# Optimization experiments

Hardware: AMD Instinct MI355X
Metric: run time of the kernel (lower is better)

The kernel has to match this reference:

```python
import jax, jax.numpy as jnp
import numpy as np

B, S, D = 8, 1024, 768
H = 12
HD = D // H  # 64


def setup_inputs() -> dict:
    key = jax.random.key(0)
    k1, k2, k3 = jax.random.split(key, 3)
    x = jax.random.normal(k1, (B, S, D), dtype=jnp.float32)
    W_qkv = jax.random.normal(k2, (D, 3 * D), dtype=jnp.float32) * (1.0 / np.sqrt(D))
    W_proj = jax.random.normal(k3, (D, D), dtype=jnp.float32) * (1.0 / np.sqrt(D))
    b_proj = jnp.zeros((D,), dtype=jnp.float32)
    return {"x": x, "W_qkv": W_qkv, "W_proj": W_proj, "b_proj": b_proj}


def reference(x, W_qkv, W_proj, b_proj):
    bs, seq, d = x.shape
    qkv = x @ W_qkv  # [B,S,3D]
    qkv = qkv.reshape(bs, seq, 3, H, HD).transpose(2, 0, 3, 1, 4)  # [3,B,H,S,HD]
    Q, K, V = qkv[0], qkv[1], qkv[2]
    scores = jnp.einsum("bhqd,bhkd->bhqk", Q, K)
    mask = jnp.triu(jnp.ones((seq, seq), dtype=bool), k=1)
    scores = jnp.where(mask, -jnp.inf, scores)
    # NOTE: original divides by d_k**(-0.5), i.e. MULTIPLIES by sqrt(HD) (faithful bug)
    weights = jax.nn.softmax(scores * np.sqrt(HD).astype(np.float32), axis=-1)
    out = jnp.einsum("bhqk,bhkd->bhqd", weights, V)  # [B,H,S,HD]
    out = out.transpose(0, 2, 1, 3).reshape(bs, seq, d)
    return out @ W_proj + b_proj
```

## Files before the change

### kernel.cpp

```cpp
#include <hip/hip_runtime.h>

typedef float f32x4 __attribute__((ext_vector_type(4)));
typedef unsigned short u16;
typedef __attribute__((ext_vector_type(8))) unsigned short u16x8;

__device__ __forceinline__ u16 f2bf(float f) {
  unsigned u = __float_as_uint(f);
  u += 0x7FFFu + ((u >> 16) & 1u);
  return (u16)(u >> 16);
}
__device__ __forceinline__ float bf2f(u16 h) { return __uint_as_float(((unsigned)h) << 16); }

__device__ __forceinline__ void mfma16(f32x4 a, f32x4 b, f32x4& c) {
  asm("v_mfma_f32_16x16x32_bf16 %0, %1, %2, %0" : "+v"(c) : "v"(a), "v"(b));
}

__device__ __forceinline__ void gload16(const u16* g, const u16* l) {
  __builtin_amdgcn_global_load_lds(
      (const __attribute__((address_space(1))) void*)g,
      (__attribute__((address_space(3))) void*)l, 16, 0, 0);
}

__device__ __forceinline__ size_t tiled_off(int r, int k) {
  return (size_t)(r >> 7) * 98304 + (size_t)(k >> 5) * 4096 +
         (size_t)((k & 31) >> 3) * 1024 + (size_t)(r & 127) * 8 + (k & 7);
}

__global__ __launch_bounds__(256) void prep_tile_x(const float* __restrict__ x,
                                                   u16* __restrict__ xh,
                                                   u16* __restrict__ xl) {
  const int lane = threadIdx.x & 63;
  const int wid = threadIdx.x >> 6;
  const int row = blockIdx.x * 64 + lane;
  const int ktile = blockIdx.y * 4 + wid;
  const float4* src = reinterpret_cast<const float4*>(x + (size_t)row * 768 + ktile * 32);
  float4 f[8];
#pragma unroll
  for (int i = 0; i < 8; ++i) f[i] = src[i];
  const size_t base = (size_t)(row >> 7) * 98304 + (size_t)ktile * 4096 + (size_t)(row & 127) * 8;
#pragma unroll
  for (int c = 0; c < 4; ++c) {
    const float v[8] = {f[2 * c].x, f[2 * c].y, f[2 * c].z, f[2 * c].w,
                        f[2 * c + 1].x, f[2 * c + 1].y, f[2 * c + 1].z, f[2 * c + 1].w};
    u16x8 h, l;
#pragma unroll
    for (int e = 0; e < 8; ++e) {
      const u16 hb = f2bf(v[e]);
      h[e] = hb;
      l[e] = f2bf(v[e] - bf2f(hb));
    }
    *(u16x8*)(xh + base + c * 1024) = h;
    *(u16x8*)(xl + base + c * 1024) = l;
  }
}

template <int WRITE_LO>
__global__ __launch_bounds__(256) void prep_wt(const float* __restrict__ W,
                                               u16* __restrict__ Wth,
                                               u16* __restrict__ Wtl, int Ncols) {
  int t = blockIdx.x * 256 + threadIdx.x;
  int total = Ncols * 192;
  if (t >= total) return;
  int n = t % Ncols;
  int k4 = t / Ncols;
  const int k0 = k4 * 4;
  u16 hh[4], ll[4];
#pragma unroll
  for (int j = 0; j < 4; ++j) {
    float v = W[(size_t)(k0 + j) * Ncols + n];
    hh[j] = f2bf(v);
    ll[j] = f2bf(v - bf2f(hh[j]));
  }
  const size_t dst = tiled_off(n, k0);
  ushort4 h4; h4.x = hh[0]; h4.y = hh[1]; h4.z = hh[2]; h4.w = hh[3];
  *reinterpret_cast<ushort4*>(Wth + dst) = h4;
  if (WRITE_LO) {
    ushort4 l4v; l4v.x = ll[0]; l4v.y = ll[1]; l4v.z = ll[2]; l4v.w = ll[3];
    *reinterpret_cast<ushort4*>(Wtl + dst) = l4v;
  }
}

template <int SPLIT>
__device__ __forceinline__ void gemm_core(u16* lds,
                                          const u16* __restrict__ Ah, const u16* __restrict__ Al,
                                          const u16* __restrict__ Bh, const u16* __restrict__ Bl,
                                          int Kdim, int rowBase, int colBase, f32x4 acc[4][4]) {
  const int tid = threadIdx.x;
  const int lane = tid & 63;
  const int wid = tid >> 6;
  const int wr = wid >> 1, wc = wid & 1;
  const int l15 = lane & 15, l4 = lane >> 4;
  const size_t aT = (size_t)(rowBase >> 7) * 98304;
  const size_t bT = (size_t)(colBase >> 7) * 98304;
  const int nk = Kdim >> 5;

  for (int kt = 0; kt < nk; ++kt) {
#pragma unroll
    for (int j = 0; j < 2; ++j) {
      const int i = wid * 2 + j;
      const size_t off = (size_t)kt * 4096 + i * 512 + lane * 8;
      gload16(Ah + aT + off, lds + i * 512);
      gload16(Bh + bT + off, lds + 4096 + i * 512);
      if constexpr (SPLIT) {
        gload16(Al + aT + off, lds + 8192 + i * 512);
        gload16(Bl + bT + off, lds + 12288 + i * 512);
      }
    }
    __syncthreads();

    f32x4 fah[4], fbh[4], fal[4], fbl[4];
#pragma unroll
    for (int mi = 0; mi < 4; ++mi) {
      const int row = wr * 64 + mi * 16 + l15;
      fah[mi] = *(const f32x4*)(lds + (l4 * 128 + row) * 8);
      if constexpr (SPLIT) fal[mi] = *(const f32x4*)(lds + 8192 + (l4 * 128 + row) * 8);
    }
#pragma unroll
    for (int nj = 0; nj < 4; ++nj) {
      const int col = wc * 64 + nj * 16 + l15;
      fbh[nj] = *(const f32x4*)(lds + 4096 + (l4 * 128 + col) * 8);
      if constexpr (SPLIT) fbl[nj] = *(const f32x4*)(lds + 12288 + (l4 * 128 + col) * 8);
    }
#pragma unroll
    for (int mi = 0; mi < 4; ++mi)
#pragma unroll
      for (int nj = 0; nj < 4; ++nj) {
        mfma16(fah[mi], fbh[nj], acc[mi][nj]);
        if constexpr (SPLIT) {
          mfma16(fah[mi], fbl[nj], acc[mi][nj]);
          mfma16(fal[mi], fbh[nj], acc[mi][nj]);
        }
      }
    __syncthreads();
  }
}

__global__ __launch_bounds__(256) void gemm_qkv_kernel(
    const u16* __restrict__ xh, const u16* __restrict__ xl,
    const u16* __restrict__ Wqh, const u16* __restrict__ Wql,
    u16* __restrict__ Qh, u16* __restrict__ Ql,
    u16* __restrict__ Kh, u16* __restrict__ Kl,
    u16* __restrict__ Vt) {
  __shared__ u16 lds[16384];
  const int rowBase = blockIdx.x * 128;
  const int colBase = blockIdx.y * 128;
  const int tid = threadIdx.x, lane = tid & 63, wid = tid >> 6;
  const int wr = wid >> 1, wc = wid & 1, l15 = lane & 15, l4 = lane >> 4;
  const int which = colBase / 768;
  const int cb = colBase % 768;

  f32x4 acc[4][4];
#pragma unroll
  for (int a = 0; a < 4; ++a)
#pragma unroll
    for (int b = 0; b < 4; ++b) acc[a][b] = (f32x4){0.f, 0.f, 0.f, 0.f};

  if (which == 2) {
    gemm_core<0>(lds, xh, nullptr, Wqh, nullptr, 768, rowBase, colBase, acc);
#pragma unroll
    for (int mi = 0; mi < 4; ++mi) {
#pragma unroll
      for (int nj = 0; nj < 4; ++nj) {
        const int crem = cb + wc * 64 + nj * 16 + l15;
        const int h = crem >> 6, d = crem & 63;
        const int rg0 = rowBase + wr * 64 + mi * 16 + l4 * 4;
        const int b = rg0 >> 10, s0 = rg0 & 1023;
        const int bh = b * 12 + h;
        ushort4 st;
        st.x = f2bf(acc[mi][nj][0]); st.y = f2bf(acc[mi][nj][1]);
        st.z = f2bf(acc[mi][nj][2]); st.w = f2bf(acc[mi][nj][3]);
        *reinterpret_cast<ushort4*>(Vt + (((size_t)(bh * 64 + d)) << 10) + s0) = st;
      }
    }
  } else {
    gemm_core<1>(lds, xh, xl, Wqh, Wql, 768, rowBase, colBase, acc);
    u16* dsth = (which == 0) ? Qh : Kh;
    u16* dstl = (which == 0) ? Ql : Kl;
#pragma unroll
    for (int mi = 0; mi < 4; ++mi) {
#pragma unroll
      for (int nj = 0; nj < 4; ++nj) {
        const int crem = cb + wc * 64 + nj * 16 + l15;
        const int h = crem >> 6, d = crem & 63;
        const int rg0 = rowBase + wr * 64 + mi * 16 + l4 * 4;
        const int b = rg0 >> 10, s0 = rg0 & 1023;
        const int bh = b * 12 + h;
#pragma unroll
        for (int r = 0; r < 4; ++r) {
          const float v = acc[mi][nj][r];
          const size_t idx = ((((size_t)bh) << 10) + s0 + r) * 64 + d;
          const u16 hb = f2bf(v);
          dsth[idx] = hb;
          dstl[idx] = f2bf(v - bf2f(hb));
        }
      }
    }
  }
}

__global__ __launch_bounds__(512, 4) void attn_kernel(
    const u16* __restrict__ Qh, const u16* __restrict__ Ql,
    const u16* __restrict__ Kh, const u16* __restrict__ Kl,
    const u16* __restrict__ Vt, u16* __restrict__ attnO) {
  const int pair = blockIdx.x;
  const int bh = blockIdx.y;
  const int tid = threadIdx.x, lane = tid & 63, w = tid >> 6;
  const int l15 = lane & 15, l4 = lane >> 4;
  __shared__ u16 kv[2][12288];
  __shared__ u16 plds[8][1024];
  u16* pl = plds[w];

  const int qt0 = pair, qt1 = 7 - pair;
  const int n0 = 2 * qt0 + 2;
  const int ntot = 18;

  const int srow = lane >> 3;
  const int schunk = (lane & 7) ^ srow;
  const int krow = w * 8 + srow;

  f32x4 qfh[2], qfl[2], o[4];
  float m[4], ls[4];

#define STAGE(BSEL, KT)                                                                   \
  do {                                                                                    \
    u16* buf_ = kv[(BSEL)];                                                               \
    const size_t kgo = (size_t)(bh * 1024 + (KT) * 64 + krow) * 64 + schunk * 8;          \
    gload16(Kh + kgo, buf_ + w * 512);                                                    \
    gload16(Kl + kgo, buf_ + 4096 + w * 512);                                             \
    gload16(Vt + (size_t)(bh * 64 + krow) * 1024 + (KT) * 64 + schunk * 8,                \
            buf_ + 8192 + w * 512);                                                       \
  } while (0)

  STAGE(0, 0);

  for (int i = 0; i < ntot; ++i) {
    const int seg = (i >= n0) ? 1 : 0;
    const int kt = seg ? (i - n0) : i;
    const int qt = seg ? qt1 : qt0;
    const int qb = qt * 128 + w * 16;
    const int nseg = seg ? (ntot - n0) : n0;

    if (i + 1 < ntot) {
      const int seg2 = (i + 1 >= n0) ? 1 : 0;
      const int kt2 = seg2 ? (i + 1 - n0) : (i + 1);
      STAGE((i + 1) & 1, kt2);
      asm volatile("s_waitcnt vmcnt(3)" ::: "memory");
    } else {
      asm volatile("s_waitcnt vmcnt(0)" ::: "memory");
    }
    __builtin_amdgcn_s_barrier();

    if (kt == 0) {
#pragma unroll
      for (int ks = 0; ks < 2; ++ks) {
        const size_t off = ((size_t)(bh * 1024 + qb + l15)) * 64 + ks * 32 + l4 * 8;
        qfh[ks] = *(const f32x4*)(Qh + off);
        qfl[ks] = *(const f32x4*)(Ql + off);
      }
#pragma unroll
      for (int n = 0; n < 4; ++n) o[n] = (f32x4){0.f, 0.f, 0.f, 0.f};
#pragma unroll
      for (int r = 0; r < 4; ++r) { m[r] = -1e30f; ls[r] = 0.f; }
    }

    if (kt * 64 <= qb + 15) {
      const u16* buf = kv[i & 1];
      f32x4 sv[4];
#pragma unroll
      for (int n = 0; n < 4; ++n) sv[n] = (f32x4){0.f, 0.f, 0.f, 0.f};
      const int rsw = l15 & 7;
#pragma unroll
      for (int nt = 0; nt < 4; ++nt) {
        const int row = nt * 16 + l15;
#pragma unroll
        for (int ks = 0; ks < 2; ++ks) {
          const int kc = ks * 4 + l4;
          const int off = row * 64 + ((kc ^ rsw) << 3);
          f32x4 kfh = *(const f32x4*)(buf + off);
          f32x4 kfl = *(const f32x4*)(buf + 4096 + off);
          mfma16(qfh[ks], kfh, sv[nt]);
          mfma16(qfh[ks], kfl, sv[nt]);
          mfma16(qfl[ks], kfh, sv[nt]);
        }
      }
      const bool diag = (kt * 64 + 63 > qb);
#pragma unroll
      for (int nt = 0; nt < 4; ++nt) {
#pragma unroll
        for (int r = 0; r < 4; ++r) {
          float xv = sv[nt][r] * 8.0f;
          if (diag) {
            const int kg = kt * 64 + nt * 16 + l15;
            const int qg = qb + l4 * 4 + r;
            if (kg > qg) xv = -1e30f;
          }
          sv[nt][r] = xv;
        }
      }
#pragma unroll
      for (int r = 0; r < 4; ++r) {
        float mx = fmaxf(fmaxf(sv[0][r], sv[1][r]), fmaxf(sv[2][r], sv[3][r]));
#pragma unroll
        for (int dd = 1; dd < 16; dd <<= 1) mx = fmaxf(mx, __shfl_xor(mx, dd));
        const float mnew = fmaxf(m[r], mx);
        const float alpha = __expf(m[r] - mnew);
        float ps = 0.f;
#pragma unroll
        for (int nt = 0; nt < 4; ++nt) {
          const float p = __expf(sv[nt][r] - mnew);
          sv[nt][r] = p;
          ps += p;
        }
#pragma unroll
        for (int dd = 1; dd < 16; dd <<= 1) ps += __shfl_xor(ps, dd);
        ls[r] = ls[r] * alpha + ps;
        m[r] = mnew;
#pragma unroll
        for (int n = 0; n < 4; ++n) o[n][r] *= alpha;
      }
#pragma unroll
      for (int nt = 0; nt < 4; ++nt) {
#pragma unroll
        for (int r = 0; r < 4; ++r) {
          const int row = l4 * 4 + r;
          const int kcol = nt * 16 + l15;
          pl[row * 64 + ((((kcol >> 3) ^ (row & 7))) << 3) + (kcol & 7)] = f2bf(sv[nt][r]);
        }
      }
#pragma unroll
      for (int ks = 0; ks < 2; ++ks) {
        const int kc = ks * 4 + l4;
        const f32x4 pa = *(const f32x4*)(pl + l15 * 64 + ((kc ^ (l15 & 7)) << 3));
#pragma unroll
        for (int nt2 = 0; nt2 < 4; ++nt2) {
          const int off = 8192 + (nt2 * 16 + l15) * 64 + ((kc ^ (l15 & 7)) << 3);
          const f32x4 vb = *(const f32x4*)(buf + off);
          mfma16(pa, vb, o[nt2]);
        }
      }
    }
    __builtin_amdgcn_s_barrier();

    if (kt == nseg - 1) {
      const int b = bh / 12, h = bh % 12;
#pragma unroll
      for (int r = 0; r < 4; ++r) {
        const float inv = 1.0f / ls[r];
        const int qg = qb + l4 * 4 + r;
        const int rowg = b * 1024 + qg;
#pragma unroll
        for (int nt2 = 0; nt2 < 4; ++nt2) {
          const int colg = h * 64 + nt2 * 16 + l15;
          attnO[tiled_off(rowg, colg)] = f2bf(o[nt2][r] * inv);
        }
      }
    }
  }
#undef STAGE
}

__global__ __launch_bounds__(256) void gemm_proj_kernel(
    const u16* __restrict__ A, const u16* __restrict__ Bt,
    const float* __restrict__ bias, float* __restrict__ out) {
  __shared__ u16 lds[8192];
  f32x4 acc[4][4];
#pragma unroll
  for (int a = 0; a < 4; ++a)
#pragma unroll
    for (int b = 0; b < 4; ++b) acc[a][b] = (f32x4){0.f, 0.f, 0.f, 0.f};

  const int rowBase = blockIdx.x * 128;
  const int colBase = blockIdx.y * 128;
  gemm_core<0>(lds, A, nullptr, Bt, nullptr, 768, rowBase, colBase, acc);

  const int tid = threadIdx.x, lane = tid & 63, wid = tid >> 6;
  const int wr = wid >> 1, wc = wid & 1, l15 = lane & 15, l4 = lane >> 4;
#pragma unroll
  for (int mi = 0; mi < 4; ++mi) {
#pragma unroll
    for (int nj = 0; nj < 4; ++nj) {
      const int cg = colBase + wc * 64 + nj * 16 + l15;
      const float bv = bias[cg];
#pragma unroll
      for (int r = 0; r < 4; ++r) {
        const int rg = rowBase + wr * 64 + mi * 16 + l4 * 4 + r;
        out[(size_t)rg * 768 + cg] = acc[mi][nj][r] + bv;
      }
    }
  }
}

extern "C" void kernel_launch(void* const* d_in, const int* in_sizes, int n_in,
                              void* d_out, int out_size, void* d_ws, size_t ws_size,
                              hipStream_t stream) {
  (void)in_sizes; (void)n_in; (void)out_size; (void)ws_size;
  const float* x = (const float*)d_in[0];
  const float* Wqkv = (const float*)d_in[1];
  const float* Wproj = (const float*)d_in[2];
  const float* bias = (const float*)d_in[3];
  float* out = (float*)d_out;
  char* ws = (char*)d_ws;

  u16* xh  = (u16*)(ws + 0);
  u16* xl  = (u16*)(ws + 12582912);
  u16* Wqh = (u16*)(ws + 25165824);
  u16* Wql = (u16*)(ws + 28704768);
  u16* Wph = (u16*)(ws + 32243712);
  u16* Qh  = (u16*)(ws + 33423360);
  u16* Ql  = (u16*)(ws + 46006272);
  u16* Kh  = (u16*)(ws + 58589184);
  u16* Kl  = (u16*)(ws + 71172096);
  u16* Vt  = (u16*)(ws + 83755008);
  u16* attn = xh;

  prep_tile_x<<<dim3(128, 6), dim3(256), 0, stream>>>(x, xh, xl);
  prep_wt<1><<<dim3(1728), dim3(256), 0, stream>>>(Wqkv, Wqh, Wql, 2304);
  prep_wt<0><<<dim3(576), dim3(256), 0, stream>>>(Wproj, Wph, (u16*)nullptr, 768);
  gemm_qkv_kernel<<<dim3(64, 18), dim3(256), 0, stream>>>(xh, xl, Wqh, Wql,
                                                          Qh, Ql, Kh, Kl, Vt);
  attn_kernel<<<dim3(4, 96), dim3(512), 0, stream>>>(Qh, Ql, Kh, Kl, Vt, attn);
  gemm_proj_kernel<<<dim3(64, 6), dim3(256), 0, stream>>>(attn, Wph, bias, out);
}
```

Measured before the change: 169.4 us.

## Transpose attention MFMA operands to keep P in registers, one q-tile per block

The attention kernel now computes S^T by swapping MFMA operand order, so each lane holds one query row. The softmax reductions become two cross-row shuffles, and P is repacked to bf16 through lane shuffles rather than staged via LDS. The paired causal q-tile scheme is replaced by one q-tile per block, launching 8x96 blocks in reverse order so the heavy tiles start first. The change also adds s_setprio around the MFMA sections and vectorized ushort4 output stores. It removes the LDS round trip and a per-block LDS buffer, at the cost of giving up the load balancing that the tile pairing provided.

Measured after the change: 184.3 us. +8.8%, slower.

```diff
diff --git a/kernel.cpp b/kernel.cpp
--- a/kernel.cpp
+++ b/kernel.cpp
@@ -2,6 +2,7 @@
 
 typedef float f32x4 __attribute__((ext_vector_type(4)));
 typedef unsigned short u16;
+typedef unsigned int u32;
 typedef __attribute__((ext_vector_type(8))) unsigned short u16x8;
 
 __device__ __forceinline__ u16 f2bf(float f) {
@@ -202,24 +203,18 @@
     const u16* __restrict__ Qh, const u16* __restrict__ Ql,
     const u16* __restrict__ Kh, const u16* __restrict__ Kl,
     const u16* __restrict__ Vt, u16* __restrict__ attnO) {
-  const int pair = blockIdx.x;
+  const int qt = 7 - blockIdx.x;
   const int bh = blockIdx.y;
   const int tid = threadIdx.x, lane = tid & 63, w = tid >> 6;
   const int l15 = lane & 15, l4 = lane >> 4;
   __shared__ u16 kv[2][12288];
-  __shared__ u16 plds[8][1024];
-  u16* pl = plds[w];
-
-  const int qt0 = pair, qt1 = 7 - pair;
-  const int n0 = 2 * qt0 + 2;
-  const int ntot = 18;
+
+  const int ntot = 2 * qt + 2;
+  const int qb = qt * 128 + w * 16;
 
   const int srow = lane >> 3;
   const int schunk = (lane & 7) ^ srow;
   const int krow = w * 8 + srow;
-
-  f32x4 qfh[2], qfl[2], o[4];
-  float m[4], ls[4];
 
 #define STAGE(BSEL, KT)                                                                   \
   do {                                                                                    \
@@ -233,42 +228,35 @@
 
   STAGE(0, 0);
 
+  f32x4 qfh[2], qfl[2];
+#pragma unroll
+  for (int ks = 0; ks < 2; ++ks) {
+    const size_t off = ((size_t)(bh * 1024 + qb + l15)) * 64 + ks * 32 + l4 * 8;
+    qfh[ks] = *(const f32x4*)(Qh + off);
+    qfl[ks] = *(const f32x4*)(Ql + off);
+  }
+  f32x4 o[4];
+#pragma unroll
+  for (int n = 0; n < 4; ++n) o[n] = (f32x4){0.f, 0.f, 0.f, 0.f};
+  float m = -1e30f, ls = 0.f;
+
   for (int i = 0; i < ntot; ++i) {
-    const int seg = (i >= n0) ? 1 : 0;
-    const int kt = seg ? (i - n0) : i;
-    const int qt = seg ? qt1 : qt0;
-    const int qb = qt * 128 + w * 16;
-    const int nseg = seg ? (ntot - n0) : n0;
-
+    const int kt = i;
     if (i + 1 < ntot) {
-      const int seg2 = (i + 1 >= n0) ? 1 : 0;
-      const int kt2 = seg2 ? (i + 1 - n0) : (i + 1);
-      STAGE((i + 1) & 1, kt2);
+      STAGE((i + 1) & 1, i + 1);
       asm volatile("s_waitcnt vmcnt(3)" ::: "memory");
     } else {
       asm volatile("s_waitcnt vmcnt(0)" ::: "memory");
     }
     __builtin_amdgcn_s_barrier();
 
-    if (kt == 0) {
-#pragma unroll
-      for (int ks = 0; ks < 2; ++ks) {
-        const size_t off = ((size_t)(bh * 1024 + qb + l15)) * 64 + ks * 32 + l4 * 8;
-        qfh[ks] = *(const f32x4*)(Qh + off);
-        qfl[ks] = *(const f32x4*)(Ql + off);
-      }
-#pragma unroll
-      for (int n = 0; n < 4; ++n) o[n] = (f32x4){0.f, 0.f, 0.f, 0.f};
-#pragma unroll
-      for (int r = 0; r < 4; ++r) { m[r] = -1e30f; ls[r] = 0.f; }
-    }
-
     if (kt * 64 <= qb + 15) {
       const u16* buf = kv[i & 1];
       f32x4 sv[4];
 #pragma unroll
       for (int n = 0; n < 4; ++n) sv[n] = (f32x4){0.f, 0.f, 0.f, 0.f};
       const int rsw = l15 & 7;
+      __builtin_amdgcn_s_setprio(1);
 #pragma unroll
       for (int nt = 0; nt < 4; ++nt) {
         const int row = nt * 16 + l15;
@@ -278,83 +266,95 @@
           const int off = row * 64 + ((kc ^ rsw) << 3);
           f32x4 kfh = *(const f32x4*)(buf + off);
           f32x4 kfl = *(const f32x4*)(buf + 4096 + off);
-          mfma16(qfh[ks], kfh, sv[nt]);
-          mfma16(qfh[ks], kfl, sv[nt]);
-          mfma16(qfl[ks], kfh, sv[nt]);
+          mfma16(kfh, qfh[ks], sv[nt]);
+          mfma16(kfh, qfl[ks], sv[nt]);
+          mfma16(kfl, qfh[ks], sv[nt]);
         }
       }
+      __builtin_amdgcn_s_setprio(0);
       const bool diag = (kt * 64 + 63 > qb);
+      const int qg = qb + l15;
 #pragma unroll
       for (int nt = 0; nt < 4; ++nt) {
 #pragma unroll
         for (int r = 0; r < 4; ++r) {
           float xv = sv[nt][r] * 8.0f;
           if (diag) {
-            const int kg = kt * 64 + nt * 16 + l15;
-            const int qg = qb + l4 * 4 + r;
+            const int kg = kt * 64 + nt * 16 + l4 * 4 + r;
             if (kg > qg) xv = -1e30f;
           }
           sv[nt][r] = xv;
         }
       }
-#pragma unroll
-      for (int r = 0; r < 4; ++r) {
-        float mx = fmaxf(fmaxf(sv[0][r], sv[1][r]), fmaxf(sv[2][r], sv[3][r]));
-#pragma unroll
-        for (int dd = 1; dd < 16; dd <<= 1) mx = fmaxf(mx, __shfl_xor(mx, dd));
-        const float mnew = fmaxf(m[r], mx);
-        const float alpha = __expf(m[r] - mnew);
-        float ps = 0.f;
-#pragma unroll
-        for (int nt = 0; nt < 4; ++nt) {
-          const float p = __expf(sv[nt][r] - mnew);
-          sv[nt][r] = p;
-          ps += p;
+      float mx = sv[0][0];
+#pragma unroll
+      for (int nt = 0; nt < 4; ++nt)
+#pragma unroll
+        for (int r = 0; r < 4; ++r) mx = fmaxf(mx, sv[nt][r]);
+      mx = fmaxf(mx, __shfl_xor(mx, 16));
+      mx = fmaxf(mx, __shfl_xor(mx, 32));
+      const float mnew = fmaxf(m, mx);
+      const float alpha = __expf(m - mnew);
+      float ps = 0.f;
+      u32 pk[4][2];
+#pragma unroll
+      for (int nt = 0; nt < 4; ++nt) {
+        float p0 = __expf(sv[nt][0] - mnew);
+        float p1 = __expf(sv[nt][1] - mnew);
+        float p2 = __expf(sv[nt][2] - mnew);
+        float p3 = __expf(sv[nt][3] - mnew);
+        ps += (p0 + p1) + (p2 + p3);
+        pk[nt][0] = (u32)f2bf(p0) | ((u32)f2bf(p1) << 16);
+        pk[nt][1] = (u32)f2bf(p2) | ((u32)f2bf(p3) << 16);
+      }
+      ps += __shfl_xor(ps, 16);
+      ps += __shfl_xor(ps, 32);
+      ls = ls * alpha + ps;
+      m = mnew;
+#pragma unroll
+      for (int n = 0; n < 4; ++n)
+#pragma unroll
+        for (int r = 0; r < 4; ++r) o[n][r] *= alpha;
+      const int srcA = l15 + ((2 * (l4 & 1)) << 4);
+      const int srcB = srcA + 16;
+      const bool sel = ((l4 >> 1) & 1) != 0;
+#pragma unroll
+      for (int ks = 0; ks < 2; ++ks) {
+        const u32 a00 = __shfl(pk[2 * ks][0], srcA), a01 = __shfl(pk[2 * ks][1], srcA);
+        const u32 a10 = __shfl(pk[2 * ks + 1][0], srcA), a11 = __shfl(pk[2 * ks + 1][1], srcA);
+        const u32 b00 = __shfl(pk[2 * ks][0], srcB), b01 = __shfl(pk[2 * ks][1], srcB);
+        const u32 b10 = __shfl(pk[2 * ks + 1][0], srcB), b11 = __shfl(pk[2 * ks + 1][1], srcB);
+        f32x4 pf;
+        pf[0] = __uint_as_float(sel ? a10 : a00);
+        pf[1] = __uint_as_float(sel ? a11 : a01);
+        pf[2] = __uint_as_float(sel ? b10 : b00);
+        pf[3] = __uint_as_float(sel ? b11 : b01);
+        const int kc = ks * 4 + l4;
+        __builtin_amdgcn_s_setprio(1);
+#pragma unroll
+        for (int nt2 = 0; nt2 < 4; ++nt2) {
+          const int off = 8192 + (nt2 * 16 + l15) * 64 + ((kc ^ rsw) << 3);
+          const f32x4 vb = *(const f32x4*)(buf + off);
+          mfma16(vb, pf, o[nt2]);
         }
-#pragma unroll
-        for (int dd = 1; dd < 16; dd <<= 1) ps += __shfl_xor(ps, dd);
-        ls[r] = ls[r] * alpha + ps;
-        m[r] = mnew;
-#pragma unroll
-        for (int n = 0; n < 4; ++n) o[n][r] *= alpha;
-      }
-#pragma unroll
-      for (int nt = 0; nt < 4; ++nt) {
-#pragma unroll
-        for (int r = 0; r < 4; ++r) {
-          const int row = l4 * 4 + r;
-          const int kcol = nt * 16 + l15;
-          pl[row * 64 + ((((kcol >> 3) ^ (row & 7))) << 3) + (kcol & 7)] = f2bf(sv[nt][r]);
-        }
-      }
-#pragma unroll
-      for (int ks = 0; ks < 2; ++ks) {
-        const int kc = ks * 4 + l4;
-        const f32x4 pa = *(const f32x4*)(pl + l15 * 64 + ((kc ^ (l15 & 7)) << 3));
-#pragma unroll
-        for (int nt2 = 0; nt2 < 4; ++nt2) {
-          const int off = 8192 + (nt2 * 16 + l15) * 64 + ((kc ^ (l15 & 7)) << 3);
-          const f32x4 vb = *(const f32x4*)(buf + off);
-          mfma16(pa, vb, o[nt2]);
-        }
+        __builtin_amdgcn_s_setprio(0);
       }
     }
     __builtin_amdgcn_s_barrier();
-
-    if (kt == nseg - 1) {
-      const int b = bh / 12, h = bh % 12;
-#pragma unroll
-      for (int r = 0; r < 4; ++r) {
-        const float inv = 1.0f / ls[r];
-        const int qg = qb + l4 * 4 + r;
-        const int rowg = b * 1024 + qg;
-#pragma unroll
-        for (int nt2 = 0; nt2 < 4; ++nt2) {
-          const int colg = h * 64 + nt2 * 16 + l15;
-          attnO[tiled_off(rowg, colg)] = f2bf(o[nt2][r] * inv);
-        }
-      }
-    }
+  }
+
+  const float inv = 1.0f / ls;
+  const int rowg = (bh / 12) * 1024 + qb + l15;
+  const int hbase = (bh % 12) * 64;
+#pragma unroll
+  for (int nt2 = 0; nt2 < 4; ++nt2) {
+    const int colg0 = hbase + nt2 * 16 + l4 * 4;
+    ushort4 st;
+    st.x = f2bf(o[nt2][0] * inv);
+    st.y = f2bf(o[nt2][1] * inv);
+    st.z = f2bf(o[nt2][2] * inv);
+    st.w = f2bf(o[nt2][3] * inv);
+    *reinterpret_cast<ushort4*>(attnO + tiled_off(rowg, colg0)) = st;
   }
 #undef STAGE
 }
@@ -418,6 +418,6 @@
   prep_wt<0><<<dim3(576), dim3(256), 0, stream>>>(Wproj, Wph, (u16*)nullptr, 768);
   gemm_qkv_kernel<<<dim3(64, 18), dim3(256), 0, stream>>>(xh, xl, Wqh, Wql,
                                                           Qh, Ql, Kh, Kl, Vt);
-  attn_kernel<<<dim3(4, 96), dim3(512), 0, stream>>>(Qh, Ql, Kh, Kl, Vt, attn);
+  attn_kernel<<<dim3(8, 96), dim3(512), 0, stream>>>(Qh, Ql, Kh, Kl, Vt, attn);
   gemm_proj_kernel<<<dim3(64, 6), dim3(256), 0, stream>>>(attn, Wph, bias, out);
 }
```
